# Kernel optimization log

Hardware: AMD Instinct MI355X
Metric: run time of the kernel (lower is better)

The kernel has to match this reference:

```python
import jax, jax.numpy as jnp
import numpy as np

NEG_SLOPE = 0.2

def setup_inputs() -> dict:
    key = jax.random.key(0)
    k1, k2, k3, k4, k5 = jax.random.split(key, 5)
    B, N, Fin, Fout, H = 4, 2048, 256, 128, 4
    h = jax.random.normal(k1, (B, N, Fin), dtype=jnp.float32)
    adj = jax.random.randint(k2, (N, N), 0, 2, dtype=jnp.int32)
    W_w = jax.random.normal(k3, (Fout, Fin), dtype=jnp.float32) * (1.414 / np.sqrt(Fin))
    W_b = jax.random.normal(k4, (Fout,), dtype=jnp.float32) * 0.01
    attn_w = jax.random.normal(k5, (H, 2 * Fout), dtype=jnp.float32) * (1.414 / np.sqrt(2 * Fout))
    return {"h": h, "adj": adj, "W_w": W_w, "W_b": W_b, "attn_w": attn_w}

def reference(h, adj, W_w, W_b, attn_w):
    Fout = W_w.shape[0]
    # Wh: [B, N, Fout]
    Wh = jnp.einsum('bnf,of->bno', h, W_w) + W_b
    a_left = attn_w[:, :Fout]   # [H, Fout]
    a_right = attn_w[:, Fout:]  # [H, Fout]
    e_left = jnp.einsum('bno,ho->bhn', Wh, a_left)   # [B, H, N]
    e_right = jnp.einsum('bno,ho->bhn', Wh, a_right)  # [B, H, N]
    # additive broadcast score: [B, H, N, N]
    e = e_left[:, :, :, None] + e_right[:, :, None, :]
    e = jnp.where(e > 0, e, NEG_SLOPE * e)  # LeakyReLU(0.2)
    mask = (adj == 0)[None, None, :, :]     # [1,1,N,N] broadcast over B,H
    e = jnp.where(mask, -jnp.inf, e)
    attn = jax.nn.softmax(e, axis=-1)
    attn = jnp.where(jnp.isnan(attn), 0.0, attn)
    # h_prime: [B, H, N, Fout]
    h_prime = jnp.einsum('bhij,bjo->bhio', attn, Wh)
    out = jnp.mean(h_prime, axis=1)
    return jax.nn.relu(out)
```

## Files before the change

### kernel.cpp

```cpp
#include <hip/hip_runtime.h>
#include <stdint.h>

#define BB 4
#define NN 2048
#define FIN 256
#define FOUT 128
#define NH 4
#define NEG_SLOPE 0.2f

typedef short bf16x8 __attribute__((ext_vector_type(8)));
typedef unsigned short u16x8 __attribute__((ext_vector_type(8)));
typedef float f32x4 __attribute__((ext_vector_type(4)));
typedef unsigned long long u64;

__device__ inline float b2f(unsigned short u) {
    union { unsigned int i; float f; } x; x.i = ((unsigned int)u) << 16; return x.f;
}
__device__ inline unsigned short f2b(float f) {
    union { float f; unsigned int i; } x; x.f = f;
    unsigned int r = x.i + 0x7fffu + ((x.i >> 16) & 1u);
    return (unsigned short)(r >> 16);
}
__device__ inline unsigned short f2b_fast(float f) {
    union { float f; unsigned int i; } x; x.f = f;
    return (unsigned short)((x.i + 0x8000u) >> 16);
}


__global__ __launch_bounds__(256) void k0_prep(const float* __restrict__ Ww,
                                               unsigned short* __restrict__ Whi,
                                               unsigned short* __restrict__ Wlo) {
    int idx = blockIdx.x * 256 + threadIdx.x;
    float v = Ww[idx];
    unsigned short hb = f2b(v);
    Whi[idx] = hb;
    Wlo[idx] = f2b(v - b2f(hb));
}

__global__ __launch_bounds__(256) void k1_wh(
    const float* __restrict__ h, const unsigned short* __restrict__ Whi,
    const unsigned short* __restrict__ Wlo, const float* __restrict__ Wb,
    const float* __restrict__ attw, unsigned short* __restrict__ WhT,
    float2* __restrict__ ELpair, float2* __restrict__ ERf,
    const int* __restrict__ adj, u64* __restrict__ mask) {
    if (blockIdx.x >= BB * NN / 16) {
        int row = blockIdx.x - BB * NN / 16;
        int wave = threadIdx.x >> 6, lane = threadIdx.x & 63;
        #pragma unroll
        for (int it = 0; it < 8; ++it) {
            int w = it * 4 + wave;
            int j = w * 64 + lane;
            u64 mm = __ballot(adj[(size_t)row * NN + j] != 0);
            if (lane == 0) mask[row * 32 + w] = mm;
        }
        return;
    }
    __shared__ unsigned short Ahi[16][264];
    __shared__ unsigned short Alo[16][264];
    __shared__ float whs[16][132];
    int t = threadIdx.x;
    int b = blockIdx.x >> 7;
    int n0 = (blockIdx.x & 127) * 16;
    {
        int r = t >> 4, c = (t & 15) * 16;
        const float* hp = h + ((size_t)(b * NN + n0 + r)) * FIN + c;
        u16x8 hi0, hi1, lo0, lo1;
        #pragma unroll
        for (int q = 0; q < 4; ++q) {
            float4 v = *(const float4*)(hp + q * 4);
            float vv[4] = {v.x, v.y, v.z, v.w};
            #pragma unroll
            for (int e = 0; e < 4; ++e) {
                int idx = q * 4 + e;
                unsigned short hb = f2b(vv[e]);
                unsigned short lb = f2b(vv[e] - b2f(hb));
                if (idx < 8) { hi0[idx] = (short)hb; lo0[idx] = (short)lb; }
                else         { hi1[idx - 8] = (short)hb; lo1[idx - 8] = (short)lb; }
            }
        }
        *(u16x8*)&Ahi[r][c] = *(u16x8*)&hi0;
        *(u16x8*)&Ahi[r][c + 8] = *(u16x8*)&hi1;
        *(u16x8*)&Alo[r][c] = *(u16x8*)&lo0;
        *(u16x8*)&Alo[r][c + 8] = *(u16x8*)&lo1;
    }
    __syncthreads();
    int lane = t & 63, wv = t >> 6;
    int m = lane & 15, quad = lane >> 4;
    int o0 = wv * 32;
    f32x4 acc0 = {0.f, 0.f, 0.f, 0.f}, acc1 = {0.f, 0.f, 0.f, 0.f};
    const unsigned short* wh0 = Whi + (size_t)(o0 + m) * FIN;
    const unsigned short* wl0 = Wlo + (size_t)(o0 + m) * FIN;
    const unsigned short* wh1 = Whi + (size_t)(o0 + 16 + m) * FIN;
    const unsigned short* wl1 = Wlo + (size_t)(o0 + 16 + m) * FIN;
    #pragma unroll
    for (int ks = 0; ks < 8; ++ks) {
        int ko = ks * 32 + quad * 8;
        bf16x8 ahi = *(bf16x8*)&Ahi[m][ko];
        bf16x8 alo = *(bf16x8*)&Alo[m][ko];
        bf16x8 bh0 = *(const bf16x8*)(wh0 + ko);
        bf16x8 bl0 = *(const bf16x8*)(wl0 + ko);
        bf16x8 bh1 = *(const bf16x8*)(wh1 + ko);
        bf16x8 bl1 = *(const bf16x8*)(wl1 + ko);
        acc0 = __builtin_amdgcn_mfma_f32_16x16x32_bf16(ahi, bh0, acc0, 0, 0, 0);
        acc0 = __builtin_amdgcn_mfma_f32_16x16x32_bf16(ahi, bl0, acc0, 0, 0, 0);
        acc0 = __builtin_amdgcn_mfma_f32_16x16x32_bf16(alo, bh0, acc0, 0, 0, 0);
        acc1 = __builtin_amdgcn_mfma_f32_16x16x32_bf16(ahi, bh1, acc1, 0, 0, 0);
        acc1 = __builtin_amdgcn_mfma_f32_16x16x32_bf16(ahi, bl1, acc1, 0, 0, 0);
        acc1 = __builtin_amdgcn_mfma_f32_16x16x32_bf16(alo, bh1, acc1, 0, 0, 0);
    }
    float bias0 = Wb[o0 + m], bias1 = Wb[o0 + 16 + m];
    #pragma unroll
    for (int reg = 0; reg < 4; ++reg) {
        int row = quad * 4 + reg;
        whs[row][o0 + m] = acc0[reg] + bias0;
        whs[row][o0 + 16 + m] = acc1[reg] + bias1;
    }
    __syncthreads();
    {
        int o = t >> 1, half = t & 1;
        u16x8 v8;
        #pragma unroll
        for (int r = 0; r < 8; ++r) v8[r] = (short)f2b(whs[half * 8 + r][o]);
        *(u16x8*)(WhT + (size_t)(b * FOUT + o) * NN + n0 + half * 8) = v8;
    }
    {
        int outi = t >> 1, half = t & 1;
        int i = outi >> 3, d = outi & 7, hh = d & 3, side = d >> 2;
        const float* arow = attw + hh * (2 * FOUT) + side * FOUT + half * 64;
        float s = 0.f;
        #pragma unroll 8
        for (int k = 0; k < 64; ++k) s = fmaf(whs[i][half * 64 + k], arow[k], s);
        s += __shfl_xor(s, 1);
        if (half == 0) {
            float p = __expf(s), n = __expf(NEG_SLOPE * s);
            if (side == 0) {
                ELpair[(size_t)(b * NH + hh) * NN + n0 + i] = make_float2(p, n);
            } else {
                ERf[((size_t)b * NN + n0 + i) * NH + hh] = make_float2(p, n);
            }
        }
    }
}

__global__ __launch_bounds__(512, 2) void k2_reg(
    const unsigned short* __restrict__ WhT, const float2* __restrict__ ERf,
    const float2* __restrict__ ELpair, const u64* __restrict__ mask,
    float* __restrict__ out) {
    __shared__ char smem[65600 + 8448 + 1536];
    float4* erf4 = (float4*)smem;
    u64* mlds = (u64*)(smem + 65600);
    float* sred = (float*)(smem + 65600 + 8448);
    int t = threadIdx.x;
    int b = blockIdx.y, i0 = blockIdx.x * 32;
    int lane = t & 63, wv = t >> 6;
    int m = lane & 15, quad = lane >> 4;
    int isub = wv & 1, kp = wv >> 1;

    {
        const float4* src = (const float4*)(ERf + (size_t)b * NN * NH);
        #pragma unroll
        for (int i = 0; i < 8; ++i) {
            int g = t + i * 512;
            erf4[g ^ (((g >> 4) & 3) << 1)] = src[g];
        }
    }
    {
        #pragma unroll
        for (int i = 0; i < 2; ++i) {
            int idx = t + i * 512;
            int r = idx >> 5, w = idx & 31;
            mlds[r * 33 + w] = mask[(size_t)(i0 + r) * 32 + w];
        }
    }
    int irow = i0 + isub * 16 + m;
    float elp[NH], eln[NH];
    #pragma unroll
    for (int hh = 0; hh < NH; ++hh) {
        float2 e2 = ELpair[(size_t)(b * NH + hh) * NN + irow];
        elp[hh] = e2.x; eln[hh] = e2.y;
    }
    __syncthreads();

    bf16x8 ones;
    #pragma unroll
    for (int e = 0; e < 8; ++e) ones[e] = (short)0x3F80;

    const unsigned short* bp[8];
    #pragma unroll
    for (int f = 0; f < 8; ++f)
        bp[f] = WhT + (size_t)(b * FOUT + f * 16 + m) * NN + kp * 32 + quad * 8;

    f32x4 acc[8][NH];
    f32x4 sacc[NH];
    #pragma unroll
    for (int f = 0; f < 8; ++f)
        #pragma unroll
        for (int hh = 0; hh < NH; ++hh) acc[f][hh] = (f32x4){0.f, 0.f, 0.f, 0.f};
    #pragma unroll
    for (int hh = 0; hh < NH; ++hh) sacc[hh] = (f32x4){0.f, 0.f, 0.f, 0.f};

    int mr = isub * 16 + m;
    int qs = quad << 1;

    for (int it = 0; it < 16; ++it) {
        int ks = (it << 2) | kp;
        int jb = ks * 32 + quad * 8;
        bf16x8 bfr[8];
        #pragma unroll
        for (int f = 0; f < 8; ++f) bfr[f] = *(const bf16x8*)(bp[f]);
        u64 w64 = mlds[mr * 33 + (ks >> 1)];
        unsigned mb = (unsigned)(w64 >> (((ks & 1) << 5) + (quad << 3))) & 0xFFu;
        int gb = jb * 2;
        bf16x8 af0, af1, af2, af3;
        #pragma unroll
        for (int e = 0; e < 8; ++e) {
            int a0 = (gb + e * 2) ^ qs;
            float4 e0 = erf4[a0];
            float4 e1 = erf4[a0 + 1];
            bool bit = (mb >> e) & 1u;
            float w0 = fmaxf(elp[0] * e0.x, eln[0] * e0.y);
            float w1 = fmaxf(elp[1] * e0.z, eln[1] * e0.w);
            float w2 = fmaxf(elp[2] * e1.x, eln[2] * e1.y);
            float w3 = fmaxf(elp[3] * e1.z, eln[3] * e1.w);
            af0[e] = bit ? (short)f2b_fast(w0) : (short)0;
            af1[e] = bit ? (short)f2b_fast(w1) : (short)0;
            af2[e] = bit ? (short)f2b_fast(w2) : (short)0;
            af3[e] = bit ? (short)f2b_fast(w3) : (short)0;
        }
        sacc[0] = __builtin_amdgcn_mfma_f32_16x16x32_bf16(af0, ones, sacc[0], 0, 0, 0);
        sacc[1] = __builtin_amdgcn_mfma_f32_16x16x32_bf16(af1, ones, sacc[1], 0, 0, 0);
        sacc[2] = __builtin_amdgcn_mfma_f32_16x16x32_bf16(af2, ones, sacc[2], 0, 0, 0);
        sacc[3] = __builtin_amdgcn_mfma_f32_16x16x32_bf16(af3, ones, sacc[3], 0, 0, 0);
        #pragma unroll
        for (int f = 0; f < 8; ++f) {
            acc[f][0] = __builtin_amdgcn_mfma_f32_16x16x32_bf16(af0, bfr[f], acc[f][0], 0, 0, 0);
            acc[f][1] = __builtin_amdgcn_mfma_f32_16x16x32_bf16(af1, bfr[f], acc[f][1], 0, 0, 0);
            acc[f][2] = __builtin_amdgcn_mfma_f32_16x16x32_bf16(af2, bfr[f], acc[f][2], 0, 0, 0);
            acc[f][3] = __builtin_amdgcn_mfma_f32_16x16x32_bf16(af3, bfr[f], acc[f][3], 0, 0, 0);
        }
        #pragma unroll
        for (int f = 0; f < 8; ++f) bp[f] += 128;
    }
    __syncthreads();

    float* red = (float*)smem;
    if (kp && m == 0) {
        #pragma unroll
        for (int hh = 0; hh < NH; ++hh)
            #pragma unroll
            for (int r = 0; r < 4; ++r)
                sred[(((kp - 1) * 2 + isub) * 16 + hh * 4 + r) * 4 + quad] = sacc[hh][r];
    }
    float v[8][4], inv[4][4];
    #pragma unroll
    for (int hh = 0; hh < NH; ++hh) {
        if (kp) {
            #pragma unroll
            for (int f = 0; f < 8; ++f)
                #pragma unroll
                for (int r = 0; r < 4; ++r)
                    red[((((kp - 1) * 2 + isub) * 8 + f) * 4 + r) * 64 + lane] = acc[f][hh][r];
        }
        __syncthreads();
        if (kp == 0) {
            if (hh == 0) {
                #pragma unroll
                for (int h2 = 0; h2 < NH; ++h2)
                    #pragma unroll
                    for (int r = 0; r < 4; ++r) {
                        float S = sacc[h2][r];
                        #pragma unroll
                        for (int k2 = 0; k2 < 3; ++k2)
                            S += sred[((k2 * 2 + isub) * 16 + h2 * 4 + r) * 4 + quad];
                        inv[h2][r] = (S > 0.f) ? 1.f / S : 0.f;
                    }
            }
            #pragma unroll
            for (int f = 0; f < 8; ++f)
                #pragma unroll
                for (int r = 0; r < 4; ++r) {
                    float tot = acc[f][hh][r];
                    #pragma unroll
                    for (int k2 = 0; k2 < 3; ++k2)
                        tot += red[(((k2 * 2 + isub) * 8 + f) * 4 + r) * 64 + lane];
                    float t2 = tot * inv[hh][r];
                    if (hh == 0) v[f][r] = t2; else v[f][r] += t2;
                }
        }
        __syncthreads();
    }
    if (kp == 0) {
        #pragma unroll
        for (int r = 0; r < 4; ++r) {
            int orow = i0 + isub * 16 + quad * 4 + r;
            #pragma unroll
            for (int f = 0; f < 8; ++f)
                out[((size_t)b * NN + orow) * FOUT + f * 16 + m] =
                    fmaxf(0.25f * v[f][r], 0.f);
        }
    }
}

extern "C" void kernel_launch(void* const* d_in, const int* in_sizes, int n_in,
                              void* d_out, int out_size, void* d_ws, size_t ws_size,
                              hipStream_t stream) {
    const float* h    = (const float*)d_in[0];
    const int* adj    = (const int*)d_in[1];
    const float* Ww   = (const float*)d_in[2];
    const float* Wb   = (const float*)d_in[3];
    const float* attw = (const float*)d_in[4];
    float* out = (float*)d_out;
    char* ws = (char*)d_ws;
    unsigned short* Whi = (unsigned short*)(ws);
    unsigned short* Wlo = (unsigned short*)(ws + 65536);
    unsigned short* WhT = (unsigned short*)(ws + 131072);
    float2*       ELpair = (float2*)(ws + 2228224);
    float2*       ERf    = (float2*)(ws + 2490368);
    u64*          mask   = (u64*)(ws + 2752512);

    k0_prep<<<dim3(128), dim3(256), 0, stream>>>(Ww, Whi, Wlo);
    k1_wh<<<dim3(BB * NN / 16 + NN), dim3(256), 0, stream>>>(h, Whi, Wlo, Wb, attw,
                                                             WhT, ELpair, ERf,
                                                             adj, mask);
    k2_reg<<<dim3(NN / 32, BB), dim3(512), 0, stream>>>(WhT, ERf, ELpair,
                                                        mask, out);
}
```

Baseline: 125.4 us.

## Pack right attention exponents as bf16 pairs and double-buffer WhT fragment loads

The right-side attention exponentials are now stored as packed bf16 pairs (one u32 per head) instead of float2, which halves the LDS staging buffer and the per-element LDS reads in the main loop. The main loop keeps two register buffers of WhT B-fragments, so the next step's global loads are issued before the current step's MFMAs. This is meant to hide global-load latency and cut LDS traffic. It costs extra VGPRs under launch_bounds(512,2), adds unpack shifts, and lowers the precision of the exponent factors to bf16.

```diff
diff --git a/kernel.cpp b/kernel.cpp
--- a/kernel.cpp
+++ b/kernel.cpp
@@ -15,6 +15,9 @@
 
 __device__ inline float b2f(unsigned short u) {
     union { unsigned int i; float f; } x; x.i = ((unsigned int)u) << 16; return x.f;
+}
+__device__ inline float asf(unsigned int u) {
+    union { unsigned int i; float f; } x; x.i = u; return x.f;
 }
 __device__ inline unsigned short f2b(float f) {
     union { float f; unsigned int i; } x; x.f = f;
@@ -41,7 +44,7 @@
     const float* __restrict__ h, const unsigned short* __restrict__ Whi,
     const unsigned short* __restrict__ Wlo, const float* __restrict__ Wb,
     const float* __restrict__ attw, unsigned short* __restrict__ WhT,
-    float2* __restrict__ ELpair, float2* __restrict__ ERf,
+    float2* __restrict__ ELpair, unsigned int* __restrict__ ERpk,
     const int* __restrict__ adj, u64* __restrict__ mask) {
     if (blockIdx.x >= BB * NN / 16) {
         int row = blockIdx.x - BB * NN / 16;
@@ -136,20 +139,52 @@
             if (side == 0) {
                 ELpair[(size_t)(b * NH + hh) * NN + n0 + i] = make_float2(p, n);
             } else {
-                ERf[((size_t)b * NN + n0 + i) * NH + hh] = make_float2(p, n);
+                ERpk[((size_t)b * NN + n0 + i) * NH + hh] =
+                    (unsigned)f2b(p) | ((unsigned)f2b(n) << 16);
             }
         }
     }
 }
 
+#define K2_STEP(BUF, KSV) do {                                                \
+    int ks_ = (KSV);                                                          \
+    int jb_ = ks_ * 32 + quad * 8;                                            \
+    u64 w64_ = mlds[mr * 33 + (ks_ >> 1)];                                    \
+    unsigned mb_ = (unsigned)(w64_ >> (((ks_ & 1) << 5) + (quad << 3))) & 0xFFu; \
+    bf16x8 af0, af1, af2, af3;                                                \
+    _Pragma("unroll")                                                         \
+    for (int e = 0; e < 8; ++e) {                                             \
+        uint4 er = erpk4[(jb_ + e) ^ (quad << 1)];                            \
+        bool bit = (mb_ >> e) & 1u;                                           \
+        float w0 = fmaxf(elp[0] * asf(er.x << 16), eln[0] * asf(er.x & 0xFFFF0000u)); \
+        float w1 = fmaxf(elp[1] * asf(er.y << 16), eln[1] * asf(er.y & 0xFFFF0000u)); \
+        float w2 = fmaxf(elp[2] * asf(er.z << 16), eln[2] * asf(er.z & 0xFFFF0000u)); \
+        float w3 = fmaxf(elp[3] * asf(er.w << 16), eln[3] * asf(er.w & 0xFFFF0000u)); \
+        af0[e] = bit ? (short)f2b_fast(w0) : (short)0;                        \
+        af1[e] = bit ? (short)f2b_fast(w1) : (short)0;                        \
+        af2[e] = bit ? (short)f2b_fast(w2) : (short)0;                        \
+        af3[e] = bit ? (short)f2b_fast(w3) : (short)0;                        \
+    }                                                                         \
+    sacc[0] = __builtin_amdgcn_mfma_f32_16x16x32_bf16(af0, ones, sacc[0], 0, 0, 0); \
+    sacc[1] = __builtin_amdgcn_mfma_f32_16x16x32_bf16(af1, ones, sacc[1], 0, 0, 0); \
+    sacc[2] = __builtin_amdgcn_mfma_f32_16x16x32_bf16(af2, ones, sacc[2], 0, 0, 0); \
+    sacc[3] = __builtin_amdgcn_mfma_f32_16x16x32_bf16(af3, ones, sacc[3], 0, 0, 0); \
+    _Pragma("unroll")                                                         \
+    for (int f = 0; f < 8; ++f) {                                             \
+        acc[f][0] = __builtin_amdgcn_mfma_f32_16x16x32_bf16(af0, BUF[f], acc[f][0], 0, 0, 0); \
+        acc[f][1] = __builtin_amdgcn_mfma_f32_16x16x32_bf16(af1, BUF[f], acc[f][1], 0, 0, 0); \
+        acc[f][2] = __builtin_amdgcn_mfma_f32_16x16x32_bf16(af2, BUF[f], acc[f][2], 0, 0, 0); \
+        acc[f][3] = __builtin_amdgcn_mfma_f32_16x16x32_bf16(af3, BUF[f], acc[f][3], 0, 0, 0); \
+    } } while (0)
+
 __global__ __launch_bounds__(512, 2) void k2_reg(
-    const unsigned short* __restrict__ WhT, const float2* __restrict__ ERf,
+    const unsigned short* __restrict__ WhT, const unsigned int* __restrict__ ERpk,
     const float2* __restrict__ ELpair, const u64* __restrict__ mask,
     float* __restrict__ out) {
-    __shared__ char smem[65600 + 8448 + 1536];
-    float4* erf4 = (float4*)smem;
-    u64* mlds = (u64*)(smem + 65600);
-    float* sred = (float*)(smem + 65600 + 8448);
+    __shared__ char smem[49152 + 1536];
+    uint4* erpk4 = (uint4*)smem;
+    u64* mlds = (u64*)(smem + 32768);
+    float* sred = (float*)(smem + 49152);
     int t = threadIdx.x;
     int b = blockIdx.y, i0 = blockIdx.x * 32;
     int lane = t & 63, wv = t >> 6;
@@ -157,11 +192,11 @@
     int isub = wv & 1, kp = wv >> 1;
 
     {
-        const float4* src = (const float4*)(ERf + (size_t)b * NN * NH);
-        #pragma unroll
-        for (int i = 0; i < 8; ++i) {
+        const uint4* src = (const uint4*)ERpk + (size_t)b * NN;
+        #pragma unroll
+        for (int i = 0; i < 4; ++i) {
             int g = t + i * 512;
-            erf4[g ^ (((g >> 4) & 3) << 1)] = src[g];
+            erpk4[g ^ (((g >> 3) & 3) << 1)] = src[g];
         }
     }
     {
@@ -200,46 +235,20 @@
     for (int hh = 0; hh < NH; ++hh) sacc[hh] = (f32x4){0.f, 0.f, 0.f, 0.f};
 
     int mr = isub * 16 + m;
-    int qs = quad << 1;
-
-    for (int it = 0; it < 16; ++it) {
-        int ks = (it << 2) | kp;
-        int jb = ks * 32 + quad * 8;
-        bf16x8 bfr[8];
-        #pragma unroll
-        for (int f = 0; f < 8; ++f) bfr[f] = *(const bf16x8*)(bp[f]);
-        u64 w64 = mlds[mr * 33 + (ks >> 1)];
-        unsigned mb = (unsigned)(w64 >> (((ks & 1) << 5) + (quad << 3))) & 0xFFu;
-        int gb = jb * 2;
-        bf16x8 af0, af1, af2, af3;
-        #pragma unroll
-        for (int e = 0; e < 8; ++e) {
-            int a0 = (gb + e * 2) ^ qs;
-            float4 e0 = erf4[a0];
-            float4 e1 = erf4[a0 + 1];
-            bool bit = (mb >> e) & 1u;
-            float w0 = fmaxf(elp[0] * e0.x, eln[0] * e0.y);
-            float w1 = fmaxf(elp[1] * e0.z, eln[1] * e0.w);
-            float w2 = fmaxf(elp[2] * e1.x, eln[2] * e1.y);
-            float w3 = fmaxf(elp[3] * e1.z, eln[3] * e1.w);
-            af0[e] = bit ? (short)f2b_fast(w0) : (short)0;
-            af1[e] = bit ? (short)f2b_fast(w1) : (short)0;
-            af2[e] = bit ? (short)f2b_fast(w2) : (short)0;
-            af3[e] = bit ? (short)f2b_fast(w3) : (short)0;
-        }
-        sacc[0] = __builtin_amdgcn_mfma_f32_16x16x32_bf16(af0, ones, sacc[0], 0, 0, 0);
-        sacc[1] = __builtin_amdgcn_mfma_f32_16x16x32_bf16(af1, ones, sacc[1], 0, 0, 0);
-        sacc[2] = __builtin_amdgcn_mfma_f32_16x16x32_bf16(af2, ones, sacc[2], 0, 0, 0);
-        sacc[3] = __builtin_amdgcn_mfma_f32_16x16x32_bf16(af3, ones, sacc[3], 0, 0, 0);
-        #pragma unroll
-        for (int f = 0; f < 8; ++f) {
-            acc[f][0] = __builtin_amdgcn_mfma_f32_16x16x32_bf16(af0, bfr[f], acc[f][0], 0, 0, 0);
-            acc[f][1] = __builtin_amdgcn_mfma_f32_16x16x32_bf16(af1, bfr[f], acc[f][1], 0, 0, 0);
-            acc[f][2] = __builtin_amdgcn_mfma_f32_16x16x32_bf16(af2, bfr[f], acc[f][2], 0, 0, 0);
-            acc[f][3] = __builtin_amdgcn_mfma_f32_16x16x32_bf16(af3, bfr[f], acc[f][3], 0, 0, 0);
-        }
-        #pragma unroll
-        for (int f = 0; f < 8; ++f) bp[f] += 128;
+
+    bf16x8 bA[8], bB[8];
+    #pragma unroll
+    for (int f = 0; f < 8; ++f) { bA[f] = *(const bf16x8*)bp[f]; bp[f] += 128; }
+    #pragma unroll 1
+    for (int it = 0; it < 16; it += 2) {
+        #pragma unroll
+        for (int f = 0; f < 8; ++f) { bB[f] = *(const bf16x8*)bp[f]; bp[f] += 128; }
+        K2_STEP(bA, (it << 2) | kp);
+        if (it + 2 < 16) {
+            #pragma unroll
+            for (int f = 0; f < 8; ++f) { bA[f] = *(const bf16x8*)bp[f]; bp[f] += 128; }
+        }
+        K2_STEP(bB, ((it + 1) << 2) | kp);
     }
     __syncthreads();
 
@@ -315,13 +324,13 @@
     unsigned short* Wlo = (unsigned short*)(ws + 65536);
     unsigned short* WhT = (unsigned short*)(ws + 131072);
     float2*       ELpair = (float2*)(ws + 2228224);
-    float2*       ERf    = (float2*)(ws + 2490368);
+    unsigned int* ERpk   = (unsigned int*)(ws + 2490368);
     u64*          mask   = (u64*)(ws + 2752512);
 
     k0_prep<<<dim3(128), dim3(256), 0, stream>>>(Ww, Whi, Wlo);
     k1_wh<<<dim3(BB * NN / 16 + NN), dim3(256), 0, stream>>>(h, Whi, Wlo, Wb, attw,
-                                                             WhT, ELpair, ERf,
+                                                             WhT, ELpair, ERpk,
                                                              adj, mask);
-    k2_reg<<<dim3(NN / 32, BB), dim3(512), 0, stream>>>(WhT, ERf, ELpair,
+    k2_reg<<<dim3(NN / 32, BB), dim3(512), 0, stream>>>(WhT, ERpk, ELpair,
                                                         mask, out);
 }
```

After: 155.2 us. 23.7% more time.
